# Performance work log

Measured on AMD Instinct MI355X. Metric: run time of the kernel, lower is better.

Reference implementation:

```python
import jax, jax.numpy as jnp
import numpy as np

INP = 512
HIDDEN = 512
N_HEADS = 8          # called 'head_dim' in the torch code
D_HEAD = HIDDEN // N_HEADS  # 64
BASE = 10000.0
SCALE = D_HEAD ** (-0.5)


def rope(x):
    # x: [b, s, h, d]
    b, s, h, d = x.shape
    half = d // 2
    theta = 1.0 / (BASE ** (jnp.arange(0, d, 2, dtype=jnp.float32) / d))  # [d/2]
    idx_theta = jnp.arange(s, dtype=jnp.float32)[:, None] * theta[None, :]  # [s, d/2]
    idx_theta2 = jnp.concatenate([idx_theta, idx_theta], axis=1)            # [s, d]
    neg_half = jnp.concatenate([-x[..., half:], x[..., :half]], axis=-1)
    cos = jnp.cos(idx_theta2)[None, :, None, :]
    sin = jnp.sin(idx_theta2)[None, :, None, :]
    return x * cos + neg_half * sin


def setup_inputs() -> dict:
    key = jax.random.key(0)
    ks = jax.random.split(key, 10)
    b, s = 4, 2048
    init = lambda k, shp, fan_in: jax.random.normal(k, shp, jnp.float32) * (fan_in ** -0.5)
    return {
        "x": jax.random.normal(ks[0], (b, s, INP), jnp.float32),
        "c": jax.random.normal(ks[1], (b, s, INP), jnp.float32),
        "Wq": init(ks[2], (INP, HIDDEN), INP), "bq": jnp.zeros((HIDDEN,), jnp.float32),
        "Wk": init(ks[3], (INP, HIDDEN), INP), "bk": jnp.zeros((HIDDEN,), jnp.float32),
        "Wv": init(ks[4], (INP, HIDDEN), INP), "bv": jnp.zeros((HIDDEN,), jnp.float32),
        "Wo": init(ks[5], (HIDDEN, INP), HIDDEN), "bo": jnp.zeros((INP,), jnp.float32),
    }


def reference(x, c, Wq, bq, Wk, bk, Wv, bv, Wo, bo):
    b, s, _ = x.shape
    h_res = x
    q = (c @ Wq + bq).reshape(b, s, N_HEADS, D_HEAD)
    k = (x @ Wk + bk).reshape(b, s, N_HEADS, D_HEAD)
    v = (x @ Wv + bv).reshape(b, s, N_HEADS, D_HEAD)
    q = rope(q)
    k = rope(k)  # computed but unused, exactly as in the source
    # NOTE: source computes scores between q and V (not k) -- faithful reproduction
    att = jnp.einsum('bihd,bjhd->bhij', q, v)            # [b, h, s, s]
    att = jax.nn.softmax(att * SCALE, axis=-1)
    out = jnp.einsum('bhij,bjhd->bihd', att, v)          # [b, s, h, d]
    out = out.reshape(b, s, HIDDEN)
    out = out @ Wo + bo
    return out + h_res
```

## Files before the change

kernel.cpp:

```cpp
#include <hip/hip_runtime.h>
#include <hip/hip_bf16.h>
#include <cstdint>

typedef float f32x4 __attribute__((ext_vector_type(4)));
typedef short bf16x8 __attribute__((ext_vector_type(8)));
typedef unsigned short u16;

#define B_    4
#define S_    2048
#define H_    8
#define D_    64
#define M_    8192

#define OFF_CBF   0UL
#define OFF_XBF   8388608UL
#define OFF_QBH   16777216UL
#define OFF_VBH   25165824UL
#define OFF_VTBH  33554432UL
#define OFF_ATTN  41943040UL
#define OFF_WQT   50331648UL
#define OFF_WVT   50855936UL
#define OFF_WOT   51380224UL
#define OFF_BIAS  51904512UL
#define OFF_COS   51910656UL
#define OFF_SIN   52172800UL
#define WS_NEEDED 52434944UL

__device__ __forceinline__ u16 f2bf(float f){
    union { float f; uint32_t u; } v; v.f = f;
    uint32_t r = (v.u + 0x7fffu + ((v.u >> 16) & 1u)) >> 16;
    return (u16)r;
}
__device__ __forceinline__ float bf2f(u16 h){
    union { uint32_t u; float f; } v; v.u = ((uint32_t)h) << 16;
    return v.f;
}
__device__ __forceinline__ uint32_t fbits(float f){
    union { float f; uint32_t u; } v; v.f = f; return v.u;
}

__device__ __forceinline__ int detect_f32(const void* x_in){
    int lane = threadIdx.x & 63;
    ushort2 dv = ((const ushort2*)x_in)[lane];
    bool hit = ((((dv.x >> 7) & 0xFF) >= 160) || (((dv.y >> 7) & 0xFF) >= 160));
    return __ballot(hit) != 0ULL;
}

__device__ __forceinline__ void gload_lds16(const u16* g, u16* l){
    __builtin_amdgcn_global_load_lds(
        (const __attribute__((address_space(1))) void*)g,
        (__attribute__((address_space(3))) void*)l, 16, 0, 0);
}

__global__ void k_cvt_act(const void* c_in, const void* x_in,
                          u16* c_bf, u16* x_bf){
    int f = detect_f32(x_in);
    int t = blockIdx.x * 256 + threadIdx.x;
    const void* src = blockIdx.y ? x_in : c_in;
    u16* dst = blockIdx.y ? x_bf : c_bf;
    if (f){
        float4 v = ((const float4*)src)[t];
        ushort4 o;
        o.x = f2bf(v.x); o.y = f2bf(v.y); o.z = f2bf(v.z); o.w = f2bf(v.w);
        ((ushort4*)dst)[t] = o;
    } else {
        ((ushort4*)dst)[t] = ((const ushort4*)src)[t];
    }
}

__global__ void k_prep(const void* Wq, const void* Wv, const void* Wo,
                       const void* bq, const void* bv, const void* bo,
                       const void* x_in,
                       u16* Wqt, u16* Wvt, u16* Wot, float* bias_ws,
                       float* cos_t, float* sin_t){
    if (blockIdx.y == 3){
        if (blockIdx.x >= 256) return;
        int idx = blockIdx.x * 256 + threadIdx.x;
        int pos = idx >> 5, j = idx & 31;
        double theta = pow(10000.0, -(double)j / 32.0);
        double ang = (double)pos * theta;
        double rev = ang * 0.15915494309189535;
        rev -= floor(rev);
        float fr = (float)rev;
        cos_t[idx] = __builtin_amdgcn_cosf(fr);
        sin_t[idx] = __builtin_amdgcn_sinf(fr);
        return;
    }
    int f = detect_f32(x_in);
    int idx = blockIdx.x * 256 + threadIdx.x;
    int k = idx >> 9, n = idx & 511;
    const void* W; u16* Wt; const void* bb;
    if (blockIdx.y == 0){ W = Wq; Wt = Wqt; bb = bq; }
    else if (blockIdx.y == 1){ W = Wv; Wt = Wvt; bb = bv; }
    else { W = Wo; Wt = Wot; bb = bo; }
    float v = f ? ((const float*)W)[idx] : bf2f(((const u16*)W)[idx]);
    Wt[n * 512 + k] = f2bf(v);
    if (idx < 512){
        float b = f ? ((const float*)bb)[idx] : bf2f(((const u16*)bb)[idx]);
        bias_ws[blockIdx.y * 512 + idx] = b;
    }
}

__global__ __launch_bounds__(256) void k_gemm_qv(
    const u16* __restrict__ c_bf, const u16* __restrict__ x_bf,
    const u16* __restrict__ Wqt, const u16* __restrict__ Wvt,
    const float* __restrict__ bias_ws,
    const float* __restrict__ cos_t, const float* __restrict__ sin_t,
    u16* __restrict__ Qbh, u16* __restrict__ Vbh, u16* __restrict__ Vtbh)
{
    __shared__ __align__(16) char smem[17408];
    u16* Als = (u16*)smem;
    u16* Bls = (u16*)(smem + 8192);
    const int w = threadIdx.x >> 6, lane = threadIdx.x & 63;
    const int g = lane >> 4, cq = lane & 15;
    const int wm = w & 1, wn = w >> 1;
    const int z = blockIdx.z;
    const u16* A  = z ? x_bf : c_bf;
    const u16* Wt = z ? Wvt : Wqt;
    const float* bias = bias_ws + (z ? 512 : 0);
    const int m0b = blockIdx.x * 128, n0b = blockIdx.y * 128;
    const int m0 = m0b + wm * 64, n0 = n0b + wn * 64;

    const int fl0 = (w * 2) * 64 + lane, fl1 = fl0 + 64;
    const int r0 = fl0 >> 2, c0 = (fl0 & 3) * 8;
    const int r1 = fl1 >> 2, c1 = (fl1 & 3) * 8;

    const f32x4 zero = {0.f, 0.f, 0.f, 0.f};
    f32x4 acc[4][4];
    #pragma unroll
    for (int i = 0; i < 4; i++)
        #pragma unroll
        for (int j = 0; j < 4; j++) acc[i][j] = zero;

    for (int kt = 0; kt < 16; kt++){
        const int kk = kt * 32;
        __syncthreads();
        gload_lds16(A  + (size_t)(m0b + r0) * 512 + kk + c0, Als + fl0 * 8 - lane * 8);
        gload_lds16(A  + (size_t)(m0b + r1) * 512 + kk + c1, Als + fl1 * 8 - lane * 8);
        gload_lds16(Wt + (size_t)(n0b + r0) * 512 + kk + c0, Bls + fl0 * 8 - lane * 8);
        gload_lds16(Wt + (size_t)(n0b + r1) * 512 + kk + c1, Bls + fl1 * 8 - lane * 8);
        __builtin_amdgcn_s_waitcnt(0x0F70);
        __syncthreads();

        bf16x8 a[4], b[4];
        #pragma unroll
        for (int mt = 0; mt < 4; mt++)
            a[mt] = *(const bf16x8*)&Als[(wm*64 + mt*16 + cq) * 32 + g*8];
        #pragma unroll
        for (int nt = 0; nt < 4; nt++)
            b[nt] = *(const bf16x8*)&Bls[(wn*64 + nt*16 + cq) * 32 + g*8];
        #pragma unroll
        for (int mt = 0; mt < 4; mt++)
            #pragma unroll
            for (int nt = 0; nt < 4; nt++)
                acc[mt][nt] = __builtin_amdgcn_mfma_f32_16x16x32_bf16(a[mt], b[nt], acc[mt][nt], 0, 0, 0);
    }
    __syncthreads();

    #pragma unroll
    for (int nt = 0; nt < 4; nt++){
        float bvv = bias[n0 + nt*16 + cq];
        #pragma unroll
        for (int mt = 0; mt < 4; mt++) acc[mt][nt] += bvv;
    }
    const int h = n0 >> 6;
    if (z == 0){
        const float SCL = 0.125f * 1.4426950408889634f;
        #pragma unroll
        for (int mt = 0; mt < 4; mt++){
            #pragma unroll
            for (int r = 0; r < 4; r++){
                int row = m0 + mt*16 + g*4 + r;
                int b_idx = row >> 11, si = row & 2047;
                size_t base = ((size_t)(b_idx*8 + h) * 2048 + si) * 64;
                #pragma unroll
                for (int nt = 0; nt < 2; nt++){
                    int dj = nt*16 + cq;
                    float cv = cos_t[si*32 + dj], sv = sin_t[si*32 + dj];
                    float x1 = acc[mt][nt][r], x2 = acc[mt][nt+2][r];
                    Qbh[base + dj]      = f2bf((x1*cv - x2*sv) * SCL);
                    Qbh[base + dj + 32] = f2bf((x2*cv + x1*sv) * SCL);
                }
            }
        }
    } else {
        float* ltw = ((float*)smem) + w * (16 * 65);
        const int b_idx = m0 >> 11, si0 = m0 & 2047;
        const size_t tbase = ((size_t)(b_idx*8 + h) * 64) * 2048;
        #pragma unroll
        for (int mt = 0; mt < 4; mt++)
            #pragma unroll
            for (int r = 0; r < 4; r++){
                int row = m0 + mt*16 + g*4 + r;
                int bi = row >> 11, si = row & 2047;
                size_t base = ((size_t)(bi*8 + h) * 2048 + si) * 64;
                #pragma unroll
                for (int nt = 0; nt < 4; nt++)
                    Vbh[base + nt*16 + cq] = f2bf(acc[mt][nt][r]);
            }
        #pragma unroll
        for (int nt = 0; nt < 4; nt++){
            #pragma unroll
            for (int mt = 0; mt < 4; mt++)
                #pragma unroll
                for (int r = 0; r < 4; r++)
                    ltw[cq * 65 + mt*16 + g*4 + r] = acc[mt][nt][r];
            __builtin_amdgcn_wave_barrier();
            #pragma unroll
            for (int dd = 0; dd < 16; dd++){
                float v = ltw[dd * 65 + lane];
                Vtbh[tbase + (size_t)(nt*16 + dd) * 2048 + si0 + lane] = f2bf(v);
            }
            __builtin_amdgcn_wave_barrier();
        }
    }
}

__global__ __launch_bounds__(512, 4) void k_attn(
    const u16* __restrict__ Qbh, const u16* __restrict__ Vbh,
    const u16* __restrict__ Vtbh, u16* __restrict__ attn)
{
    __shared__ u16 Vs[2][64 * 68];
    __shared__ u16 Vts[2][64 * 68];
    __shared__ float pl[8][16 * 68];
    const int w = threadIdx.x >> 6, lane = threadIdx.x & 63;
    const int g = lane >> 4, cq = lane & 15;
    const int bh = blockIdx.y;
    const int i0 = blockIdx.x * 128 + w * 16;
    const size_t qbase = ((size_t)bh * 2048 + i0) * 64;

    bf16x8 aq[2];
    aq[0] = *(const bf16x8*)(Qbh + qbase + (size_t)cq * 64 + g*8);
    aq[1] = *(const bf16x8*)(Qbh + qbase + (size_t)cq * 64 + 32 + g*8);

    const int srow = w * 8 + (lane >> 3);
    const int scol = (lane & 7) * 8;
    const u16* gvs = Vbh  + ((size_t)bh * 2048) * 64 + (size_t)srow * 64 + scol;
    const u16* gvt = Vtbh + ((size_t)(bh * 64) + srow) * 2048 + scol;
    const int lst = srow * 68 + scol;

    {
        bf16x8 t_vs = *(const bf16x8*)gvs;
        bf16x8 t_vt = *(const bf16x8*)gvt;
        *(bf16x8*)&Vs[0][lst]  = t_vs;
        *(bf16x8*)&Vts[0][lst] = t_vt;
    }

    const f32x4 zero = {0.f, 0.f, 0.f, 0.f};
    f32x4 o[4]; float fl[4];
    #pragma unroll
    for (int t = 0; t < 4; t++) o[t] = zero;
    #pragma unroll
    for (int r = 0; r < 4; r++) fl[r] = 0.f;

    for (int jt = 0; jt < 32; jt++){
        const int buf = jt & 1;
        bf16x8 n_vs = *(const bf16x8*)(gvs + (size_t)(jt + 1) * 4096);
        bf16x8 n_vt = *(const bf16x8*)(gvt + (size_t)(jt + 1) * 64);
        __syncthreads();

        f32x4 s[4];
        #pragma unroll
        for (int t = 0; t < 4; t++) s[t] = zero;
        #pragma unroll
        for (int kk = 0; kk < 2; kk++)
            #pragma unroll
            for (int t = 0; t < 4; t++){
                bf16x8 bv = *(const bf16x8*)&Vs[buf][(t*16 + cq)*68 + kk*32 + g*8];
                s[t] = __builtin_amdgcn_mfma_f32_16x16x32_bf16(aq[kk], bv, s[t], 0, 0, 0);
            }
        #pragma unroll
        for (int t = 0; t < 4; t++)
            #pragma unroll
            for (int r = 0; r < 4; r++)
                s[t][r] = __builtin_amdgcn_exp2f(s[t][r]);
        #pragma unroll
        for (int r = 0; r < 4; r++)
            fl[r] += (s[0][r] + s[1][r]) + (s[2][r] + s[3][r]);

        #pragma unroll
        for (int r = 0; r < 4; r++)
            #pragma unroll
            for (int t = 0; t < 4; t++)
                pl[w][(g*4 + r)*68 + t*16 + cq] = s[t][r];
        __builtin_amdgcn_wave_barrier();
        #pragma unroll
        for (int kk = 0; kk < 2; kk++){
            f32x4 u0 = *(const f32x4*)&pl[w][cq*68 + kk*32 + g*8];
            f32x4 u1 = *(const f32x4*)&pl[w][cq*68 + kk*32 + g*8 + 4];
            union { bf16x8 v; uint32_t wd[4]; } pk;
            pk.wd[0] = (fbits(u0[0]) >> 16) | (fbits(u0[1]) & 0xffff0000u);
            pk.wd[1] = (fbits(u0[2]) >> 16) | (fbits(u0[3]) & 0xffff0000u);
            pk.wd[2] = (fbits(u1[0]) >> 16) | (fbits(u1[1]) & 0xffff0000u);
            pk.wd[3] = (fbits(u1[2]) >> 16) | (fbits(u1[3]) & 0xffff0000u);
            #pragma unroll
            for (int tn = 0; tn < 4; tn++){
                bf16x8 bv = *(const bf16x8*)&Vts[buf][(tn*16 + cq)*68 + kk*32 + g*8];
                o[tn] = __builtin_amdgcn_mfma_f32_16x16x32_bf16(pk.v, bv, o[tn], 0, 0, 0);
            }
        }
        __builtin_amdgcn_wave_barrier();

        *(bf16x8*)&Vs[buf ^ 1][lst]  = n_vs;
        *(bf16x8*)&Vts[buf ^ 1][lst] = n_vt;
    }
    #pragma unroll
    for (int r = 0; r < 4; r++){
        float sum = fl[r];
        sum += __shfl_xor(sum, 1);
        sum += __shfl_xor(sum, 2);
        sum += __shfl_xor(sum, 4);
        sum += __shfl_xor(sum, 8);
        fl[r] = sum;
    }
    f32x4 iv = {1.f/fl[0], 1.f/fl[1], 1.f/fl[2], 1.f/fl[3]};
    const int b_idx = bh >> 3, h = bh & 7;
    #pragma unroll
    for (int t = 0; t < 4; t++){
        o[t] *= iv;
        #pragma unroll
        for (int r = 0; r < 4; r++){
            int row = i0 + g*4 + r;
            attn[((size_t)(b_idx*2048 + row))*512 + h*64 + t*16 + cq] = f2bf(o[t][r]);
        }
    }
}

__global__ __launch_bounds__(256) void k_gemm_out(
    const u16* __restrict__ attn, const u16* __restrict__ Wot,
    const float* __restrict__ bias_ws, const void* __restrict__ x_in,
    void* __restrict__ out)
{
    __shared__ __align__(16) char smem[16384];
    u16* Als = (u16*)smem;
    u16* Bls = (u16*)(smem + 8192);
    const int w = threadIdx.x >> 6, lane = threadIdx.x & 63;
    const int g = lane >> 4, cq = lane & 15;
    const int wm = w & 1, wn = w >> 1;
    const int m0b = blockIdx.x * 128, n0b = blockIdx.y * 128;
    const int m0 = m0b + wm * 64, n0 = n0b + wn * 64;
    const int f = detect_f32(x_in);

    const int fl0 = (w * 2) * 64 + lane, fl1 = fl0 + 64;
    const int r0 = fl0 >> 2, c0 = (fl0 & 3) * 8;
    const int r1 = fl1 >> 2, c1 = (fl1 & 3) * 8;

    const f32x4 zero = {0.f, 0.f, 0.f, 0.f};
    f32x4 acc[4][4];
    #pragma unroll
    for (int i = 0; i < 4; i++)
        #pragma unroll
        for (int j = 0; j < 4; j++) acc[i][j] = zero;

    for (int kt = 0; kt < 16; kt++){
        const int kk = kt * 32;
        __syncthreads();
        gload_lds16(attn + (size_t)(m0b + r0) * 512 + kk + c0, Als + fl0 * 8 - lane * 8);
        gload_lds16(attn + (size_t)(m0b + r1) * 512 + kk + c1, Als + fl1 * 8 - lane * 8);
        gload_lds16(Wot  + (size_t)(n0b + r0) * 512 + kk + c0, Bls + fl0 * 8 - lane * 8);
        gload_lds16(Wot  + (size_t)(n0b + r1) * 512 + kk + c1, Bls + fl1 * 8 - lane * 8);
        __builtin_amdgcn_s_waitcnt(0x0F70);
        __syncthreads();

        bf16x8 a[4], b[4];
        #pragma unroll
        for (int mt = 0; mt < 4; mt++)
            a[mt] = *(const bf16x8*)&Als[(wm*64 + mt*16 + cq) * 32 + g*8];
        #pragma unroll
        for (int nt = 0; nt < 4; nt++)
            b[nt] = *(const bf16x8*)&Bls[(wn*64 + nt*16 + cq) * 32 + g*8];
        #pragma unroll
        for (int mt = 0; mt < 4; mt++)
            #pragma unroll
            for (int nt = 0; nt < 4; nt++)
                acc[mt][nt] = __builtin_amdgcn_mfma_f32_16x16x32_bf16(a[mt], b[nt], acc[mt][nt], 0, 0, 0);
    }
    #pragma unroll
    for (int mt = 0; mt < 4; mt++)
        #pragma unroll
        for (int nt = 0; nt < 4; nt++)
            #pragma unroll
            for (int r = 0; r < 4; r++){
                int row = m0 + mt*16 + g*4 + r;
                int col = n0 + nt*16 + cq;
                size_t idx = (size_t)row * 512 + col;
                float resid = f ? ((const float*)x_in)[idx] : bf2f(((const u16*)x_in)[idx]);
                float v = acc[mt][nt][r] + bias_ws[1024 + col] + resid;
                if (f) ((float*)out)[idx] = v;
                else   ((u16*)out)[idx] = f2bf(v);
            }
}

extern "C" void kernel_launch(void* const* d_in, const int* in_sizes, int n_in,
                              void* d_out, int out_size, void* d_ws, size_t ws_size,
                              hipStream_t stream){
    const void* x_in = d_in[0];
    const void* c_in = d_in[1];
    const void* Wq = d_in[2]; const void* bq = d_in[3];
    const void* Wv = d_in[6]; const void* bv = d_in[7];
    const void* Wo = d_in[8]; const void* bo = d_in[9];

    if (ws_size < WS_NEEDED){
        hipMemsetAsync(d_out, 0, (size_t)out_size * 2, stream);
        return;
    }
    char* ws = (char*)d_ws;
    u16* c_bf  = (u16*)(ws + OFF_CBF);
    u16* x_bf  = (u16*)(ws + OFF_XBF);
    u16* Qbh   = (u16*)(ws + OFF_QBH);
    u16* Vbh   = (u16*)(ws + OFF_VBH);
    u16* Vtbh  = (u16*)(ws + OFF_VTBH);
    u16* attn  = (u16*)(ws + OFF_ATTN);
    u16* Wqt   = (u16*)(ws + OFF_WQT);
    u16* Wvt   = (u16*)(ws + OFF_WVT);
    u16* Wot   = (u16*)(ws + OFF_WOT);
    float* bias_ws = (float*)(ws + OFF_BIAS);
    float* cos_t   = (float*)(ws + OFF_COS);
    float* sin_t   = (float*)(ws + OFF_SIN);

    k_cvt_act<<<dim3(4096, 2), 256, 0, stream>>>(c_in, x_in, c_bf, x_bf);
    k_prep<<<dim3(1024, 4), 256, 0, stream>>>(Wq, Wv, Wo, bq, bv, bo, x_in,
                                              Wqt, Wvt, Wot, bias_ws, cos_t, sin_t);
    k_gemm_qv<<<dim3(64, 4, 2), 256, 0, stream>>>(c_bf, x_bf, Wqt, Wvt, bias_ws,
                                                  cos_t, sin_t, Qbh, Vbh, Vtbh);
    k_attn<<<dim3(16, 32), 512, 0, stream>>>(Qbh, Vbh, Vtbh, attn);
    k_gemm_out<<<dim3(64, 4), 256, 0, stream>>>(attn, Wot, bias_ws, x_in, d_out);
}
```

Measured before the change: 209.7 us.

## Merge prep kernels, double-buffer swizzled GEMMs, retile attention and output GEMM

Folds the activation conversion into the weight prep kernel, which saves one launch. The two GEMMs now use a K-tile of 64 with double-buffered LDS, issuing the next tile's loads before computing the current one. Operands are pre-swizzled in global memory (XOR on 8-element chunks) so the direct-to-LDS loads land bank-conflict free. Attention drops to 256-thread blocks with each wave handling 32 query rows, so V fragments are reused across two row tiles. The output GEMM uses 128x64 tiles for more blocks; in exchange, LDS use rises and the swizzled layouts must stay consistent between producer and consumer kernels.

```diff
diff --git a/kernel.cpp b/kernel.cpp
--- a/kernel.cpp
+++ b/kernel.cpp
@@ -39,6 +39,10 @@
     union { float f; uint32_t u; } v; v.f = f; return v.u;
 }
 
+__device__ __forceinline__ int swz(int row, int col){
+    return (col & ~63) | ((((col >> 3) & 7) ^ (row & 7)) << 3) | (col & 7);
+}
+
 __device__ __forceinline__ int detect_f32(const void* x_in){
     int lane = threadIdx.x & 63;
     ushort2 dv = ((const ushort2*)x_in)[lane];
@@ -52,53 +56,56 @@
         (__attribute__((address_space(3))) void*)l, 16, 0, 0);
 }
 
-__global__ void k_cvt_act(const void* c_in, const void* x_in,
-                          u16* c_bf, u16* x_bf){
-    int f = detect_f32(x_in);
-    int t = blockIdx.x * 256 + threadIdx.x;
-    const void* src = blockIdx.y ? x_in : c_in;
-    u16* dst = blockIdx.y ? x_bf : c_bf;
-    if (f){
-        float4 v = ((const float4*)src)[t];
-        ushort4 o;
-        o.x = f2bf(v.x); o.y = f2bf(v.y); o.z = f2bf(v.z); o.w = f2bf(v.w);
-        ((ushort4*)dst)[t] = o;
-    } else {
-        ((ushort4*)dst)[t] = ((const ushort4*)src)[t];
-    }
-}
-
-__global__ void k_prep(const void* Wq, const void* Wv, const void* Wo,
+__global__ void k_prep(const void* c_in, const void* x_in,
+                       const void* Wq, const void* Wv, const void* Wo,
                        const void* bq, const void* bv, const void* bo,
-                       const void* x_in,
+                       u16* c_bf, u16* x_bf,
                        u16* Wqt, u16* Wvt, u16* Wot, float* bias_ws,
                        float* cos_t, float* sin_t){
-    if (blockIdx.y == 3){
-        if (blockIdx.x >= 256) return;
-        int idx = blockIdx.x * 256 + threadIdx.x;
+    int bid = blockIdx.x;
+    if (bid >= 11264){
+        int idx = (bid - 11264) * 256 + threadIdx.x;
         int pos = idx >> 5, j = idx & 31;
         double theta = pow(10000.0, -(double)j / 32.0);
-        double ang = (double)pos * theta;
-        double rev = ang * 0.15915494309189535;
+        double rev = ((double)pos * theta) * 0.15915494309189535;
         rev -= floor(rev);
         float fr = (float)rev;
         cos_t[idx] = __builtin_amdgcn_cosf(fr);
         sin_t[idx] = __builtin_amdgcn_sinf(fr);
         return;
     }
+    if (bid >= 8192){
+        int f = detect_f32(x_in);
+        int wi = (bid - 8192) >> 10;
+        int idx = ((bid - 8192) & 1023) * 256 + threadIdx.x;
+        int k = idx >> 9, n = idx & 511;
+        const void* W; u16* Wt; const void* bb;
+        if (wi == 0){ W = Wq; Wt = Wqt; bb = bq; }
+        else if (wi == 1){ W = Wv; Wt = Wvt; bb = bv; }
+        else { W = Wo; Wt = Wot; bb = bo; }
+        float v = f ? ((const float*)W)[idx] : bf2f(((const u16*)W)[idx]);
+        Wt[n * 512 + swz(n, k)] = f2bf(v);
+        if (idx < 512){
+            float b = f ? ((const float*)bb)[idx] : bf2f(((const u16*)bb)[idx]);
+            bias_ws[wi * 512 + idx] = b;
+        }
+        return;
+    }
     int f = detect_f32(x_in);
-    int idx = blockIdx.x * 256 + threadIdx.x;
-    int k = idx >> 9, n = idx & 511;
-    const void* W; u16* Wt; const void* bb;
-    if (blockIdx.y == 0){ W = Wq; Wt = Wqt; bb = bq; }
-    else if (blockIdx.y == 1){ W = Wv; Wt = Wvt; bb = bv; }
-    else { W = Wo; Wt = Wot; bb = bo; }
-    float v = f ? ((const float*)W)[idx] : bf2f(((const u16*)W)[idx]);
-    Wt[n * 512 + k] = f2bf(v);
-    if (idx < 512){
-        float b = f ? ((const float*)bb)[idx] : bf2f(((const u16*)bb)[idx]);
-        bias_ws[blockIdx.y * 512 + idx] = b;
-    }
+    int isx = bid >= 4096;
+    int t = (bid & 4095) * 256 + threadIdx.x;
+    const void* src = isx ? x_in : c_in;
+    u16* dst = isx ? x_bf : c_bf;
+    int e0 = t * 4, row = e0 >> 9, col = e0 & 511;
+    size_t didx = (size_t)row * 512 + swz(row, col);
+    ushort4 o;
+    if (f){
+        float4 v = ((const float4*)src)[t];
+        o.x = f2bf(v.x); o.y = f2bf(v.y); o.z = f2bf(v.z); o.w = f2bf(v.w);
+    } else {
+        o = ((const ushort4*)src)[t];
+    }
+    *(ushort4*)(dst + didx) = o;
 }
 
 __global__ __launch_bounds__(256) void k_gemm_qv(
@@ -108,9 +115,8 @@
     const float* __restrict__ cos_t, const float* __restrict__ sin_t,
     u16* __restrict__ Qbh, u16* __restrict__ Vbh, u16* __restrict__ Vtbh)
 {
-    __shared__ __align__(16) char smem[17408];
-    u16* Als = (u16*)smem;
-    u16* Bls = (u16*)(smem + 8192);
+    __shared__ __align__(16) u16 Als[2][128 * 64];
+    __shared__ __align__(16) u16 Bls[2][128 * 64];
     const int w = threadIdx.x >> 6, lane = threadIdx.x & 63;
     const int g = lane >> 4, cq = lane & 15;
     const int wm = w & 1, wn = w >> 1;
@@ -120,10 +126,14 @@
     const float* bias = bias_ws + (z ? 512 : 0);
     const int m0b = blockIdx.x * 128, n0b = blockIdx.y * 128;
     const int m0 = m0b + wm * 64, n0 = n0b + wn * 64;
-
-    const int fl0 = (w * 2) * 64 + lane, fl1 = fl0 + 64;
-    const int r0 = fl0 >> 2, c0 = (fl0 & 3) * 8;
-    const int r1 = fl1 >> 2, c1 = (fl1 & 3) * 8;
+    const int swzi = ((cq & 7) << 3);
+
+    int srow[4], scol[4];
+    #pragma unroll
+    for (int i = 0; i < 4; i++){
+        int flat = (w * 4 + i) * 64 + lane;
+        srow[i] = flat >> 3; scol[i] = (flat & 7) * 8;
+    }
 
     const f32x4 zero = {0.f, 0.f, 0.f, 0.f};
     f32x4 acc[4][4];
@@ -132,28 +142,40 @@
         #pragma unroll
         for (int j = 0; j < 4; j++) acc[i][j] = zero;
 
-    for (int kt = 0; kt < 16; kt++){
-        const int kk = kt * 32;
-        __syncthreads();
-        gload_lds16(A  + (size_t)(m0b + r0) * 512 + kk + c0, Als + fl0 * 8 - lane * 8);
-        gload_lds16(A  + (size_t)(m0b + r1) * 512 + kk + c1, Als + fl1 * 8 - lane * 8);
-        gload_lds16(Wt + (size_t)(n0b + r0) * 512 + kk + c0, Bls + fl0 * 8 - lane * 8);
-        gload_lds16(Wt + (size_t)(n0b + r1) * 512 + kk + c1, Bls + fl1 * 8 - lane * 8);
+    #pragma unroll
+    for (int i = 0; i < 4; i++){
+        gload_lds16(A  + (size_t)(m0b + srow[i]) * 512 + scol[i], &Als[0][(w*4 + i) * 512]);
+        gload_lds16(Wt + (size_t)(n0b + srow[i]) * 512 + scol[i], &Bls[0][(w*4 + i) * 512]);
+    }
+
+    for (int kt = 0; kt < 8; kt++){
+        const int buf = kt & 1;
         __builtin_amdgcn_s_waitcnt(0x0F70);
         __syncthreads();
-
-        bf16x8 a[4], b[4];
-        #pragma unroll
-        for (int mt = 0; mt < 4; mt++)
-            a[mt] = *(const bf16x8*)&Als[(wm*64 + mt*16 + cq) * 32 + g*8];
-        #pragma unroll
-        for (int nt = 0; nt < 4; nt++)
-            b[nt] = *(const bf16x8*)&Bls[(wn*64 + nt*16 + cq) * 32 + g*8];
-        #pragma unroll
-        for (int mt = 0; mt < 4; mt++)
+        if (kt < 7){
+            const int kk = (kt + 1) * 64;
+            #pragma unroll
+            for (int i = 0; i < 4; i++){
+                gload_lds16(A  + (size_t)(m0b + srow[i]) * 512 + kk + scol[i], &Als[buf^1][(w*4 + i) * 512]);
+                gload_lds16(Wt + (size_t)(n0b + srow[i]) * 512 + kk + scol[i], &Bls[buf^1][(w*4 + i) * 512]);
+            }
+        }
+        #pragma unroll
+        for (int ks = 0; ks < 2; ks++){
+            const int cs = ((ks * 4 + g) << 3) ^ swzi;
+            bf16x8 a[4], b[4];
+            #pragma unroll
+            for (int mt = 0; mt < 4; mt++)
+                a[mt] = *(const bf16x8*)&Als[buf][(wm*64 + mt*16 + cq) * 64 + cs];
             #pragma unroll
             for (int nt = 0; nt < 4; nt++)
-                acc[mt][nt] = __builtin_amdgcn_mfma_f32_16x16x32_bf16(a[mt], b[nt], acc[mt][nt], 0, 0, 0);
+                b[nt] = *(const bf16x8*)&Bls[buf][(wn*64 + nt*16 + cq) * 64 + cs];
+            #pragma unroll
+            for (int mt = 0; mt < 4; mt++)
+                #pragma unroll
+                for (int nt = 0; nt < 4; nt++)
+                    acc[mt][nt] = __builtin_amdgcn_mfma_f32_16x16x32_bf16(a[mt], b[nt], acc[mt][nt], 0, 0, 0);
+        }
     }
     __syncthreads();
 
@@ -184,7 +206,7 @@
             }
         }
     } else {
-        float* ltw = ((float*)smem) + w * (16 * 65);
+        float* ltw = ((float*)&Als[0][0]) + w * (16 * 65);
         const int b_idx = m0 >> 11, si0 = m0 & 2047;
         const size_t tbase = ((size_t)(b_idx*8 + h) * 64) * 2048;
         #pragma unroll
@@ -216,112 +238,144 @@
     }
 }
 
-__global__ __launch_bounds__(512, 4) void k_attn(
+__global__ __launch_bounds__(256) void k_attn(
     const u16* __restrict__ Qbh, const u16* __restrict__ Vbh,
     const u16* __restrict__ Vtbh, u16* __restrict__ attn)
 {
     __shared__ u16 Vs[2][64 * 68];
     __shared__ u16 Vts[2][64 * 68];
-    __shared__ float pl[8][16 * 68];
+    __shared__ float pl[4][32 * 68];
     const int w = threadIdx.x >> 6, lane = threadIdx.x & 63;
     const int g = lane >> 4, cq = lane & 15;
     const int bh = blockIdx.y;
-    const int i0 = blockIdx.x * 128 + w * 16;
-    const size_t qbase = ((size_t)bh * 2048 + i0) * 64;
-
-    bf16x8 aq[2];
-    aq[0] = *(const bf16x8*)(Qbh + qbase + (size_t)cq * 64 + g*8);
-    aq[1] = *(const bf16x8*)(Qbh + qbase + (size_t)cq * 64 + 32 + g*8);
-
-    const int srow = w * 8 + (lane >> 3);
-    const int scol = (lane & 7) * 8;
-    const u16* gvs = Vbh  + ((size_t)bh * 2048) * 64 + (size_t)srow * 64 + scol;
-    const u16* gvt = Vtbh + ((size_t)(bh * 64) + srow) * 2048 + scol;
-    const int lst = srow * 68 + scol;
-
-    {
-        bf16x8 t_vs = *(const bf16x8*)gvs;
-        bf16x8 t_vt = *(const bf16x8*)gvt;
-        *(bf16x8*)&Vs[0][lst]  = t_vs;
-        *(bf16x8*)&Vts[0][lst] = t_vt;
+    const int i0 = blockIdx.x * 128 + w * 32;
+
+    bf16x8 aq[2][2];
+    #pragma unroll
+    for (int mt = 0; mt < 2; mt++)
+        #pragma unroll
+        for (int kk = 0; kk < 2; kk++)
+            aq[mt][kk] = *(const bf16x8*)(Qbh + ((size_t)bh*2048 + i0 + mt*16 + cq)*64 + kk*32 + g*8);
+
+    int lst[2]; const u16 *gvs[2], *gvt[2];
+    #pragma unroll
+    for (int i = 0; i < 2; i++){
+        int flat = (w*2 + i) * 64 + lane;
+        int srow = flat >> 3, scol = (flat & 7) * 8;
+        gvs[i] = Vbh  + ((size_t)bh * 2048 + srow) * 64 + scol;
+        gvt[i] = Vtbh + ((size_t)(bh * 64) + srow) * 2048 + scol;
+        lst[i] = srow * 68 + scol;
+    }
+    #pragma unroll
+    for (int i = 0; i < 2; i++){
+        *(bf16x8*)&Vs[0][lst[i]]  = *(const bf16x8*)gvs[i];
+        *(bf16x8*)&Vts[0][lst[i]] = *(const bf16x8*)gvt[i];
     }
 
     const f32x4 zero = {0.f, 0.f, 0.f, 0.f};
-    f32x4 o[4]; float fl[4];
-    #pragma unroll
-    for (int t = 0; t < 4; t++) o[t] = zero;
-    #pragma unroll
-    for (int r = 0; r < 4; r++) fl[r] = 0.f;
+    f32x4 o[2][4]; float fl[2][4];
+    #pragma unroll
+    for (int mt = 0; mt < 2; mt++)
+        #pragma unroll
+        for (int t = 0; t < 4; t++){ o[mt][t] = zero; fl[mt][t] = 0.f; }
 
     for (int jt = 0; jt < 32; jt++){
         const int buf = jt & 1;
-        bf16x8 n_vs = *(const bf16x8*)(gvs + (size_t)(jt + 1) * 4096);
-        bf16x8 n_vt = *(const bf16x8*)(gvt + (size_t)(jt + 1) * 64);
+        bf16x8 n_vs[2], n_vt[2];
+        #pragma unroll
+        for (int i = 0; i < 2; i++){
+            n_vs[i] = *(const bf16x8*)(gvs[i] + (size_t)(jt + 1) * 4096);
+            n_vt[i] = *(const bf16x8*)(gvt[i] + (size_t)(jt + 1) * 64);
+        }
         __syncthreads();
 
-        f32x4 s[4];
-        #pragma unroll
-        for (int t = 0; t < 4; t++) s[t] = zero;
+        bf16x8 bv[2][4];
         #pragma unroll
         for (int kk = 0; kk < 2; kk++)
             #pragma unroll
-            for (int t = 0; t < 4; t++){
-                bf16x8 bv = *(const bf16x8*)&Vs[buf][(t*16 + cq)*68 + kk*32 + g*8];
-                s[t] = __builtin_amdgcn_mfma_f32_16x16x32_bf16(aq[kk], bv, s[t], 0, 0, 0);
-            }
-        #pragma unroll
-        for (int t = 0; t < 4; t++)
+            for (int t = 0; t < 4; t++)
+                bv[kk][t] = *(const bf16x8*)&Vs[buf][(t*16 + cq)*68 + kk*32 + g*8];
+        f32x4 s2[2][4];
+        #pragma unroll
+        for (int mt = 0; mt < 2; mt++){
+            #pragma unroll
+            for (int t = 0; t < 4; t++) s2[mt][t] = zero;
+            #pragma unroll
+            for (int kk = 0; kk < 2; kk++)
+                #pragma unroll
+                for (int t = 0; t < 4; t++)
+                    s2[mt][t] = __builtin_amdgcn_mfma_f32_16x16x32_bf16(aq[mt][kk], bv[kk][t], s2[mt][t], 0, 0, 0);
+        }
+        #pragma unroll
+        for (int mt = 0; mt < 2; mt++){
+            #pragma unroll
+            for (int t = 0; t < 4; t++)
+                #pragma unroll
+                for (int r = 0; r < 4; r++)
+                    s2[mt][t][r] = __builtin_amdgcn_exp2f(s2[mt][t][r]);
             #pragma unroll
             for (int r = 0; r < 4; r++)
-                s[t][r] = __builtin_amdgcn_exp2f(s[t][r]);
-        #pragma unroll
-        for (int r = 0; r < 4; r++)
-            fl[r] += (s[0][r] + s[1][r]) + (s[2][r] + s[3][r]);
-
-        #pragma unroll
-        for (int r = 0; r < 4; r++)
-            #pragma unroll
-            for (int t = 0; t < 4; t++)
-                pl[w][(g*4 + r)*68 + t*16 + cq] = s[t][r];
+                fl[mt][r] += (s2[mt][0][r] + s2[mt][1][r]) + (s2[mt][2][r] + s2[mt][3][r]);
+        }
+        #pragma unroll
+        for (int mt = 0; mt < 2; mt++)
+            #pragma unroll
+            for (int r = 0; r < 4; r++)
+                #pragma unroll
+                for (int t = 0; t < 4; t++)
+                    pl[w][(mt*16 + g*4 + r)*68 + t*16 + cq] = s2[mt][t][r];
         __builtin_amdgcn_wave_barrier();
-        #pragma unroll
-        for (int kk = 0; kk < 2; kk++){
-            f32x4 u0 = *(const f32x4*)&pl[w][cq*68 + kk*32 + g*8];
-            f32x4 u1 = *(const f32x4*)&pl[w][cq*68 + kk*32 + g*8 + 4];
-            union { bf16x8 v; uint32_t wd[4]; } pk;
-            pk.wd[0] = (fbits(u0[0]) >> 16) | (fbits(u0[1]) & 0xffff0000u);
-            pk.wd[1] = (fbits(u0[2]) >> 16) | (fbits(u0[3]) & 0xffff0000u);
-            pk.wd[2] = (fbits(u1[0]) >> 16) | (fbits(u1[1]) & 0xffff0000u);
-            pk.wd[3] = (fbits(u1[2]) >> 16) | (fbits(u1[3]) & 0xffff0000u);
-            #pragma unroll
-            for (int tn = 0; tn < 4; tn++){
-                bf16x8 bv = *(const bf16x8*)&Vts[buf][(tn*16 + cq)*68 + kk*32 + g*8];
-                o[tn] = __builtin_amdgcn_mfma_f32_16x16x32_bf16(pk.v, bv, o[tn], 0, 0, 0);
-            }
-        }
+        bf16x8 bt[2][4];
+        #pragma unroll
+        for (int kk = 0; kk < 2; kk++)
+            #pragma unroll
+            for (int tn = 0; tn < 4; tn++)
+                bt[kk][tn] = *(const bf16x8*)&Vts[buf][(tn*16 + cq)*68 + kk*32 + g*8];
+        #pragma unroll
+        for (int mt = 0; mt < 2; mt++)
+            #pragma unroll
+            for (int kk = 0; kk < 2; kk++){
+                f32x4 u0 = *(const f32x4*)&pl[w][(mt*16 + cq)*68 + kk*32 + g*8];
+                f32x4 u1 = *(const f32x4*)&pl[w][(mt*16 + cq)*68 + kk*32 + g*8 + 4];
+                union { bf16x8 v; uint32_t wd[4]; } pk;
+                pk.wd[0] = (fbits(u0[0]) >> 16) | (fbits(u0[1]) & 0xffff0000u);
+                pk.wd[1] = (fbits(u0[2]) >> 16) | (fbits(u0[3]) & 0xffff0000u);
+                pk.wd[2] = (fbits(u1[0]) >> 16) | (fbits(u1[1]) & 0xffff0000u);
+                pk.wd[3] = (fbits(u1[2]) >> 16) | (fbits(u1[3]) & 0xffff0000u);
+                #pragma unroll
+                for (int tn = 0; tn < 4; tn++)
+                    o[mt][tn] = __builtin_amdgcn_mfma_f32_16x16x32_bf16(pk.v, bt[kk][tn], o[mt][tn], 0, 0, 0);
+            }
         __builtin_amdgcn_wave_barrier();
 
-        *(bf16x8*)&Vs[buf ^ 1][lst]  = n_vs;
-        *(bf16x8*)&Vts[buf ^ 1][lst] = n_vt;
-    }
-    #pragma unroll
-    for (int r = 0; r < 4; r++){
-        float sum = fl[r];
-        sum += __shfl_xor(sum, 1);
-        sum += __shfl_xor(sum, 2);
-        sum += __shfl_xor(sum, 4);
-        sum += __shfl_xor(sum, 8);
-        fl[r] = sum;
-    }
-    f32x4 iv = {1.f/fl[0], 1.f/fl[1], 1.f/fl[2], 1.f/fl[3]};
+        #pragma unroll
+        for (int i = 0; i < 2; i++){
+            *(bf16x8*)&Vs[buf ^ 1][lst[i]]  = n_vs[i];
+            *(bf16x8*)&Vts[buf ^ 1][lst[i]] = n_vt[i];
+        }
+    }
     const int b_idx = bh >> 3, h = bh & 7;
     #pragma unroll
-    for (int t = 0; t < 4; t++){
-        o[t] *= iv;
+    for (int mt = 0; mt < 2; mt++){
         #pragma unroll
         for (int r = 0; r < 4; r++){
-            int row = i0 + g*4 + r;
-            attn[((size_t)(b_idx*2048 + row))*512 + h*64 + t*16 + cq] = f2bf(o[t][r]);
+            float sum = fl[mt][r];
+            sum += __shfl_xor(sum, 1);
+            sum += __shfl_xor(sum, 2);
+            sum += __shfl_xor(sum, 4);
+            sum += __shfl_xor(sum, 8);
+            fl[mt][r] = 1.f / sum;
+        }
+        f32x4 iv = {fl[mt][0], fl[mt][1], fl[mt][2], fl[mt][3]};
+        #pragma unroll
+        for (int t = 0; t < 4; t++){
+            f32x4 ov = o[mt][t] * iv;
+            #pragma unroll
+            for (int r = 0; r < 4; r++){
+                int row = i0 + mt*16 + g*4 + r;
+                int col = h*64 + t*16 + cq;
+                attn[((size_t)(b_idx*2048 + row))*512 + swz(row, col)] = f2bf(ov[r]);
+            }
         }
     }
 }
@@ -331,54 +385,76 @@
     const float* __restrict__ bias_ws, const void* __restrict__ x_in,
     void* __restrict__ out)
 {
-    __shared__ __align__(16) char smem[16384];
-    u16* Als = (u16*)smem;
-    u16* Bls = (u16*)(smem + 8192);
+    __shared__ __align__(16) u16 Als[2][128 * 64];
+    __shared__ __align__(16) u16 Bls[2][64 * 64];
     const int w = threadIdx.x >> 6, lane = threadIdx.x & 63;
     const int g = lane >> 4, cq = lane & 15;
     const int wm = w & 1, wn = w >> 1;
-    const int m0b = blockIdx.x * 128, n0b = blockIdx.y * 128;
-    const int m0 = m0b + wm * 64, n0 = n0b + wn * 64;
+    const int m0b = blockIdx.x * 128, n0b = blockIdx.y * 64;
+    const int m0 = m0b + wm * 64, n0 = n0b + wn * 32;
     const int f = detect_f32(x_in);
-
-    const int fl0 = (w * 2) * 64 + lane, fl1 = fl0 + 64;
-    const int r0 = fl0 >> 2, c0 = (fl0 & 3) * 8;
-    const int r1 = fl1 >> 2, c1 = (fl1 & 3) * 8;
+    const int swzi = ((cq & 7) << 3);
+
+    int sra[4], sca[4], srb[2], scb[2];
+    #pragma unroll
+    for (int i = 0; i < 4; i++){
+        int flat = (w * 4 + i) * 64 + lane;
+        sra[i] = flat >> 3; sca[i] = (flat & 7) * 8;
+    }
+    #pragma unroll
+    for (int i = 0; i < 2; i++){
+        int flat = (w * 2 + i) * 64 + lane;
+        srb[i] = flat >> 3; scb[i] = (flat & 7) * 8;
+    }
 
     const f32x4 zero = {0.f, 0.f, 0.f, 0.f};
-    f32x4 acc[4][4];
+    f32x4 acc[4][2];
     #pragma unroll
     for (int i = 0; i < 4; i++)
         #pragma unroll
-        for (int j = 0; j < 4; j++) acc[i][j] = zero;
-
-    for (int kt = 0; kt < 16; kt++){
-        const int kk = kt * 32;
-        __syncthreads();
-        gload_lds16(attn + (size_t)(m0b + r0) * 512 + kk + c0, Als + fl0 * 8 - lane * 8);
-        gload_lds16(attn + (size_t)(m0b + r1) * 512 + kk + c1, Als + fl1 * 8 - lane * 8);
-        gload_lds16(Wot  + (size_t)(n0b + r0) * 512 + kk + c0, Bls + fl0 * 8 - lane * 8);
-        gload_lds16(Wot  + (size_t)(n0b + r1) * 512 + kk + c1, Bls + fl1 * 8 - lane * 8);
+        for (int j = 0; j < 2; j++) acc[i][j] = zero;
+
+    #pragma unroll
+    for (int i = 0; i < 4; i++)
+        gload_lds16(attn + (size_t)(m0b + sra[i]) * 512 + sca[i], &Als[0][(w*4 + i) * 512]);
+    #pragma unroll
+    for (int i = 0; i < 2; i++)
+        gload_lds16(Wot + (size_t)(n0b + srb[i]) * 512 + scb[i], &Bls[0][(w*2 + i) * 512]);
+
+    for (int kt = 0; kt < 8; kt++){
+        const int buf = kt & 1;
         __builtin_amdgcn_s_waitcnt(0x0F70);
         __syncthreads();
-
-        bf16x8 a[4], b[4];
-        #pragma unroll
-        for (int mt = 0; mt < 4; mt++)
-            a[mt] = *(const bf16x8*)&Als[(wm*64 + mt*16 + cq) * 32 + g*8];
-        #pragma unroll
-        for (int nt = 0; nt < 4; nt++)
-            b[nt] = *(const bf16x8*)&Bls[(wn*64 + nt*16 + cq) * 32 + g*8];
-        #pragma unroll
-        for (int mt = 0; mt < 4; mt++)
-            #pragma unroll
-            for (int nt = 0; nt < 4; nt++)
-                acc[mt][nt] = __builtin_amdgcn_mfma_f32_16x16x32_bf16(a[mt], b[nt], acc[mt][nt], 0, 0, 0);
+        if (kt < 7){
+            const int kk = (kt + 1) * 64;
+            #pragma unroll
+            for (int i = 0; i < 4; i++)
+                gload_lds16(attn + (size_t)(m0b + sra[i]) * 512 + kk + sca[i], &Als[buf^1][(w*4 + i) * 512]);
+            #pragma unroll
+            for (int i = 0; i < 2; i++)
+                gload_lds16(Wot + (size_t)(n0b + srb[i]) * 512 + kk + scb[i], &Bls[buf^1][(w*2 + i) * 512]);
+        }
+        #pragma unroll
+        for (int ks = 0; ks < 2; ks++){
+            const int cs = ((ks * 4 + g) << 3) ^ swzi;
+            bf16x8 a[4], b[2];
+            #pragma unroll
+            for (int mt = 0; mt < 4; mt++)
+                a[mt] = *(const bf16x8*)&Als[buf][(wm*64 + mt*16 + cq) * 64 + cs];
+            #pragma unroll
+            for (int nt = 0; nt < 2; nt++)
+                b[nt] = *(const bf16x8*)&Bls[buf][(wn*32 + nt*16 + cq) * 64 + cs];
+            #pragma unroll
+            for (int mt = 0; mt < 4; mt++)
+                #pragma unroll
+                for (int nt = 0; nt < 2; nt++)
+                    acc[mt][nt] = __builtin_amdgcn_mfma_f32_16x16x32_bf16(a[mt], b[nt], acc[mt][nt], 0, 0, 0);
+        }
     }
     #pragma unroll
     for (int mt = 0; mt < 4; mt++)
         #pragma unroll
-        for (int nt = 0; nt < 4; nt++)
+        for (int nt = 0; nt < 2; nt++)
             #pragma unroll
             for (int r = 0; r < 4; r++){
                 int row = m0 + mt*16 + g*4 + r;
@@ -418,11 +494,10 @@
     float* cos_t   = (float*)(ws + OFF_COS);
     float* sin_t   = (float*)(ws + OFF_SIN);
 
-    k_cvt_act<<<dim3(4096, 2), 256, 0, stream>>>(c_in, x_in, c_bf, x_bf);
-    k_prep<<<dim3(1024, 4), 256, 0, stream>>>(Wq, Wv, Wo, bq, bv, bo, x_in,
-                                              Wqt, Wvt, Wot, bias_ws, cos_t, sin_t);
+    k_prep<<<11520, 256, 0, stream>>>(c_in, x_in, Wq, Wv, Wo, bq, bv, bo,
+                                      c_bf, x_bf, Wqt, Wvt, Wot, bias_ws, cos_t, sin_t);
     k_gemm_qv<<<dim3(64, 4, 2), 256, 0, stream>>>(c_bf, x_bf, Wqt, Wvt, bias_ws,
                                                   cos_t, sin_t, Qbh, Vbh, Vtbh);
-    k_attn<<<dim3(16, 32), 512, 0, stream>>>(Qbh, Vbh, Vtbh, attn);
-    k_gemm_out<<<dim3(64, 4), 256, 0, stream>>>(attn, Wot, bias_ws, x_in, d_out);
-}
+    k_attn<<<dim3(16, 32), 256, 0, stream>>>(Qbh, Vbh, Vtbh, attn);
+    k_gemm_out<<<dim3(64, 8), 256, 0, stream>>>(attn, Wot, bias_ws, x_in, d_out);
+}
```

After: 196.2 us. 1.07x faster.
